# Kernel optimization log

Measured on AMD Instinct MI355X. Metric: run time of the kernel, lower is better.

## Reference

```python
import jax, jax.numpy as jnp
import numpy as np

B, S, D = 2, 2048, 4096
NH, NKV = 32, 8
HD = D // NH          # 128
NREP = NH // NKV      # 4
SCALE = HD ** -0.5


def setup_inputs() -> dict:
    key = jax.random.key(0)
    kx, kq, kk, kv, ko = jax.random.split(key, 5)
    s = 0.02
    return {
        "x": jax.random.normal(kx, (B, S, D), dtype=jnp.float32),
        "wq": jax.random.normal(kq, (D, NH * HD), dtype=jnp.float32) * s,
        "wk": jax.random.normal(kk, (D, NKV * HD), dtype=jnp.float32) * s,
        "wv": jax.random.normal(kv, (D, NKV * HD), dtype=jnp.float32) * s,
        "wo": jax.random.normal(ko, (NH * HD, D), dtype=jnp.float32) * s,
    }


def reference(x, wq, wk, wv, wo):
    b, s, _ = x.shape
    q = (x @ wq).reshape(b, s, NH, HD)    # b s h d
    k = (x @ wk).reshape(b, s, NKV, HD)   # b s kv d
    v = (x @ wv).reshape(b, s, NKV, HD)
    # GQA: repeat kv heads to match query heads
    k = jnp.repeat(k, NREP, axis=2)       # b s h d
    v = jnp.repeat(v, NREP, axis=2)
    scores = jnp.einsum("bihd,bjhd->bhij", q, k) * SCALE  # b h i j
    causal = jnp.tril(jnp.ones((s, s), dtype=bool))
    scores = jnp.where(causal, scores, jnp.finfo(scores.dtype).min)
    attn = jax.nn.softmax(scores, axis=-1)
    out = jnp.einsum("bhij,bjhd->bihd", attn, v)          # b s h d
    out = out.reshape(b, s, NH * HD)
    return out @ wo
```

## Files before the change

kernel.cpp:

```cpp
#include <hip/hip_runtime.h>
#include <cstdint>
#include <cstddef>

typedef __bf16 bf16x8 __attribute__((ext_vector_type(8)));
typedef float  f32x4  __attribute__((ext_vector_type(4)));
typedef unsigned short u16;

#define SCALE_F 0.08838834764831845f
#define QSCALE_F (0.08838834764831845f * 1.4426950408889634f)

__device__ __forceinline__ u16 f2bf(float f) {
  unsigned int u = __builtin_bit_cast(unsigned int, f);
  u += 0x7fffu + ((u >> 16) & 1u);
  return (u16)(u >> 16);
}

__device__ __forceinline__ unsigned cvt_pk_bf16(float lo, float hi) {
  unsigned r;
  asm("v_cvt_pk_bf16_f32 %0, %1, %2" : "=v"(r) : "v"(lo), "v"(hi));
  return r;
}

__device__ __forceinline__ void load_lds16(const void* g, void* l) {
  __builtin_amdgcn_global_load_lds((const __attribute__((address_space(1))) void*)g,
                                   (__attribute__((address_space(3))) void*)l,
                                   16, 0, 0);
}

__global__ __launch_bounds__(256) void prep_all(const float* __restrict__ x,
                                                const float* __restrict__ wq,
                                                const float* __restrict__ wk,
                                                const float* __restrict__ wv,
                                                const float* __restrict__ wo,
                                                u16* __restrict__ xb,
                                                u16* __restrict__ wqT,
                                                u16* __restrict__ wkvT,
                                                u16* __restrict__ woT) {
  __shared__ float tile[64][33];
  const int tid = threadIdx.x;
  int blk = blockIdx.x;
  if (blk < 2048) {
    int idx = blk * 256 + tid;
    const int n4 = 4096 * 4096 / 4;
    for (; idx < n4; idx += 2048 * 256) {
      float4 v = ((const float4*)x)[idx];
      uint2 pk;
      pk.x = (unsigned)f2bf(v.x) | ((unsigned)f2bf(v.y) << 16);
      pk.y = (unsigned)f2bf(v.z) | ((unsigned)f2bf(v.w) << 16);
      ((uint2*)xb)[idx] = pk;
    }
    return;
  }
  blk -= 2048;
  const float* in; u16* out; long C; int nbx; float scale;
  if (blk < 8192)       { in = wq; out = wqT;                           C = 4096; nbx = 128; scale = QSCALE_F; }
  else if (blk < 10240) { blk -= 8192;  in = wk; out = wkvT;                          C = 1024; nbx = 32; scale = 1.f; }
  else if (blk < 12288) { blk -= 10240; in = wv; out = wkvT + (size_t)1024 * 4096;    C = 1024; nbx = 32; scale = 1.f; }
  else                  { blk -= 12288; in = wo; out = woT;                           C = 4096; nbx = 128; scale = 1.f; }
  const long R = 4096;
  const long c0 = (long)(blk % nbx) * 32, r0 = (long)(blk / nbx) * 64;
  {
    const int tx = tid & 31, ty = tid >> 5;
#pragma unroll
    for (int i = 0; i < 8; i++)
      tile[ty + i * 8][tx] = in[(r0 + ty + i * 8) * C + c0 + tx];
  }
  __syncthreads();
  {
    const int tx = tid & 31, cy = tid >> 5;
#pragma unroll
    for (int i = 0; i < 4; i++) {
      int col = cy + i * 8;
      unsigned val = (unsigned)f2bf(tile[2 * tx][col] * scale) |
                     ((unsigned)f2bf(tile[2 * tx + 1][col] * scale) << 16);
      *(unsigned*)&out[(c0 + col) * R + r0 + 2 * tx] = val;
    }
  }
}

__global__ __launch_bounds__(256) void transpose_u16(const u16* __restrict__ in,
                                                     u16* __restrict__ out,
                                                     int R, int C, int ldi, int ldo) {
  __shared__ u16 tile[32][33];
  const int tx = threadIdx.x, ty = threadIdx.y;
  const long c0 = (long)blockIdx.x * 32, r0 = (long)blockIdx.y * 32;
#pragma unroll
  for (int i = 0; i < 4; i++)
    tile[ty + i * 8][tx] = in[(r0 + ty + i * 8) * (long)ldi + c0 + tx];
  __syncthreads();
#pragma unroll
  for (int i = 0; i < 4; i++)
    out[(c0 + ty + i * 8) * (long)ldo + r0 + tx] = tile[tx][ty + i * 8];
}

__global__ __launch_bounds__(256) void reduce_kv(const float* __restrict__ part,
                                                 u16* __restrict__ kvb, int n4) {
  int idx = blockIdx.x * 256 + threadIdx.x;
  const int stride = gridDim.x * 256;
  const float4* p0 = (const float4*)part;
  const float4* p1 = (const float4*)(part + (size_t)4096 * 2048);
  for (; idx < n4; idx += stride) {
    float4 a = p0[idx], b = p1[idx];
    uint2 pk;
    pk.x = (unsigned)f2bf(a.x + b.x) | ((unsigned)f2bf(a.y + b.y) << 16);
    pk.y = (unsigned)f2bf(a.z + b.z) | ((unsigned)f2bf(a.w + b.w) << 16);
    ((uint2*)kvb)[idx] = pk;
  }
}

#define STGA(db, ks, KC) { int kc_ = (KC) < K ? (KC) : 0; \
    load_lds16(gA0 + kc_, &SA[db][ks][s0 * 8]); \
    load_lds16(gA1 + kc_, &SA[db][ks][s1 * 8]); }
#define STGB(db, ks, KC) { int kc_ = (KC) < K ? (KC) : 0; \
    load_lds16(gB0 + kc_, &SB[db][ks][s0 * 8]); \
    load_lds16(gB1 + kc_, &SB[db][ks][s1 * 8]); }

#define PH(MBc, AU, BU, DBn, KSn, MBn, AN, RDB, BN_, STG, DOVM) { \
    STG; \
    if (DOVM) asm volatile("s_waitcnt vmcnt(8)"); \
    __builtin_amdgcn_s_barrier(); \
    _Pragma("unroll") for (int mm = 0; mm < 4; mm++) \
      AN[mm] = *(const bf16x8*)(&SA[DBn][KSn][aoff + (MBn + mm) * 512]); \
    if (RDB) { \
      _Pragma("unroll") for (int n = 0; n < 4; n++) \
        BN_[n] = *(const bf16x8*)(&SB[DBn][KSn][boff + n * 512]); \
    } \
    __builtin_amdgcn_s_setprio(1); \
    _Pragma("unroll") for (int mm = 0; mm < 4; mm++) \
      _Pragma("unroll") for (int n = 0; n < 4; n++) \
        acc[MBc + mm][n] = __builtin_amdgcn_mfma_f32_16x16x32_bf16(AU[mm], BU[n], acc[MBc + mm][n], 0, 0, 0); \
    __builtin_amdgcn_s_setprio(0); \
  }

template <int BF16_OUT>
__device__ __forceinline__ void gemm_core(const u16* __restrict__ A,
                                          const u16* __restrict__ Bt,
                                          void* __restrict__ Cv,
                                          long bm, long bn,
                                          int N, int K, int lda, int ldb) {
  __shared__ u16 SA[2][2][8192];
  __shared__ u16 SB[2][2][8192];
  const int tid = threadIdx.x;
  const int lane = tid & 63;
  const int g = lane >> 4, r16 = lane & 15;
  const int wid = tid >> 6;
  const int wm = wid >> 2, wn = wid & 3;

  const int s0 = tid, s1 = 512 + tid;
  const int rp0 = s0 >> 3, ci0 = (s0 & 7) ^ (rp0 & 7);
  const int rp1 = s1 >> 3, ci1 = (s1 & 7) ^ (rp1 & 7);
  const long gr0 = rp0 * 2 + (ci0 >> 2), gc0 = (ci0 & 3) * 8;
  const long gr1 = rp1 * 2 + (ci1 >> 2), gc1 = (ci1 & 3) * 8;
  const u16* gA0 = A + (bm + gr0) * lda + gc0;
  const u16* gA1 = A + (bm + gr1) * lda + gc1;
  const u16* gB0 = Bt + (bn + gr0) * ldb + gc0;
  const u16* gB1 = Bt + (bn + gr1) * ldb + gc1;

  const int rA = wm * 128 + r16;
  const int aoff = (rA >> 1) * 64 + ((((rA & 1) << 2) + g) ^ ((rA >> 1) & 7)) * 8;
  const int rB = wn * 64 + r16;
  const int boff = (rB >> 1) * 64 + ((((rB & 1) << 2) + g) ^ ((rB >> 1) & 7)) * 8;

  f32x4 acc[8][4];
#pragma unroll
  for (int m = 0; m < 8; m++)
#pragma unroll
    for (int n = 0; n < 4; n++)
#pragma unroll
      for (int j = 0; j < 4; j++) acc[m][n][j] = 0.f;

  bf16x8 afrX[4], afrY[4], bfrX[4], bfrY[4];

  STGA(0, 0, 0); STGB(0, 0, 0);
  STGA(0, 1, 32); STGB(0, 1, 32);
  STGA(1, 0, 64); STGB(1, 0, 64);
  __builtin_amdgcn_sched_barrier(0);
  asm volatile("s_waitcnt vmcnt(0)" ::: "memory");
  __builtin_amdgcn_s_barrier();

#pragma unroll
  for (int mm = 0; mm < 4; mm++)
    afrX[mm] = *(const bf16x8*)(&SA[0][0][aoff + mm * 512]);
#pragma unroll
  for (int n = 0; n < 4; n++)
    bfrX[n] = *(const bf16x8*)(&SB[0][0][boff + n * 512]);

  for (int it = 0; it < K / 128; it++) {
    const int t0 = it * 128;
    PH(0, afrX, bfrX, 0, 0, 4, afrY, 0, bfrY, STGA(1, 1, t0 + 96), 0);
    PH(4, afrY, bfrX, 0, 1, 0, afrX, 1, bfrY, STGB(1, 1, t0 + 96), 1);
    PH(0, afrX, bfrY, 0, 1, 4, afrY, 0, bfrX, STGA(0, 0, t0 + 128), 0);
    PH(4, afrY, bfrY, 1, 0, 0, afrX, 1, bfrX, STGB(0, 0, t0 + 128), 1);
    PH(0, afrX, bfrX, 1, 0, 4, afrY, 0, bfrY, STGA(0, 1, t0 + 160), 0);
    PH(4, afrY, bfrX, 1, 1, 0, afrX, 1, bfrY, STGB(0, 1, t0 + 160), 1);
    PH(0, afrX, bfrY, 1, 1, 4, afrY, 0, bfrX, STGA(1, 0, t0 + 192), 0);
    PH(4, afrY, bfrY, 0, 0, 0, afrX, 1, bfrX, STGB(1, 0, t0 + 192), 1);
  }

  const long crow = bm + wm * 128 + g * 4;
  const long ccol = bn + wn * 64 + r16;
  if (BF16_OUT) {
    u16* C = (u16*)Cv;
#pragma unroll
    for (int m = 0; m < 8; m++)
#pragma unroll
      for (int n = 0; n < 4; n++)
#pragma unroll
        for (int j = 0; j < 4; j++)
          C[(crow + m * 16 + j) * (long)N + ccol + n * 16] = f2bf(acc[m][n][j]);
  } else {
    float* C = (float*)Cv;
#pragma unroll
    for (int m = 0; m < 8; m++)
#pragma unroll
      for (int n = 0; n < 4; n++)
#pragma unroll
        for (int j = 0; j < 4; j++)
          C[(crow + m * 16 + j) * (long)N + ccol + n * 16] = acc[m][n][j];
  }
}

__global__ __launch_bounds__(512, 2) void gemm_q(const u16* __restrict__ A,
                                                 const u16* __restrict__ Bt,
                                                 void* __restrict__ Cv) {
  const int cpx = gridDim.x >> 3;
  const int lin = ((int)blockIdx.x & 7) * cpx + ((int)blockIdx.x >> 3);
  gemm_core<1>(A, Bt, Cv, (long)(lin / 16) * 256, (long)(lin % 16) * 256,
               4096, 4096, 4096, 4096);
}

__global__ __launch_bounds__(512, 2) void gemm_kv(const u16* __restrict__ A,
                                                  const u16* __restrict__ Bt,
                                                  float* __restrict__ part) {
  const int cpx = gridDim.x >> 3;
  const int lin = ((int)blockIdx.x & 7) * cpx + ((int)blockIdx.x >> 3);
  const int sk = lin >> 7;
  const int t = lin & 127;
  gemm_core<0>(A + sk * 2048, Bt + sk * 2048,
               part + (size_t)sk * 4096 * 2048,
               (long)(t >> 3) * 256, (long)(t & 7) * 256,
               2048, 2048, 4096, 4096);
}

__global__ __launch_bounds__(512, 2) void gemm_wo(const u16* __restrict__ A,
                                                  const u16* __restrict__ Bt,
                                                  void* __restrict__ Cv) {
  const int cpx = gridDim.x >> 3;
  const int lin = ((int)blockIdx.x & 7) * cpx + ((int)blockIdx.x >> 3);
  gemm_core<0>(A, Bt, Cv, (long)(lin / 16) * 256, (long)(lin % 16) * 256,
               4096, 4096, 4096, 4096);
}

#define ATILE(CUR, I, PREF) do { \
    const int kt_ = ((I) < nktA) ? (I) : (I) - nktA; \
    const int kb_ = kt_ * 64; \
    if (PREF) { \
      const int in_ = (I) + 1; \
      const int ktn_ = (in_ < nktA) ? in_ : in_ - nktA; \
      stage(CUR ^ 1, ktn_ * 64); \
    } \
    if (kb_ <= qlo + 15) { \
      const bool masked_ = (kb_ + 63 > qlo); \
      f32x4 st[4]; \
      _Pragma("unroll") for (int t = 0; t < 4; t++) \
        _Pragma("unroll") for (int j = 0; j < 4; j++) st[t][j] = 0.f; \
      _Pragma("unroll") for (int t = 0; t < 4; t++) \
        _Pragma("unroll") for (int kc = 0; kc < 4; kc++) { \
          bf16x8 kf = *(const bf16x8*)(kaK[CUR][kc & 1] + t * 2048 + (kc >> 1) * 64); \
          st[t] = __builtin_amdgcn_mfma_f32_16x16x32_bf16(kf, qf[kc], st[t], 0, 0, 0); \
        } \
      float p[4][4], tm[4]; \
      _Pragma("unroll") for (int t = 0; t < 4; t++) { \
        _Pragma("unroll") for (int j = 0; j < 4; j++) { \
          float s = st[t][j]; \
          if (masked_) { \
            int kv = kb_ + t * 16 + g * 4 + j; \
            s = (kv > qrow) ? -__builtin_inff() : s; \
          } \
          p[t][j] = s; \
        } \
        tm[t] = fmaxf(fmaxf(p[t][0], p[t][1]), fmaxf(p[t][2], p[t][3])); \
      } \
      float tmax = fmaxf(fmaxf(tm[0], tm[1]), fmaxf(tm[2], tm[3])); \
      tmax = fmaxf(tmax, __shfl_xor(tmax, 16)); \
      tmax = fmaxf(tmax, __shfl_xor(tmax, 32)); \
      if (!__all(tmax <= mrun + 8.f)) { \
        const float mnew = fmaxf(mrun, tmax); \
        const float esc = exp2f(mrun - mnew); \
        float es[4]; \
        _Pragma("unroll") for (int j = 0; j < 4; j++) es[j] = __shfl(esc, (lane & 48) + g * 4 + j); \
        _Pragma("unroll") for (int dt = 0; dt < 8; dt++) \
          _Pragma("unroll") for (int j = 0; j < 4; j++) oacc[dt][j] *= es[j]; \
        lrun *= esc; \
        mrun = mnew; \
      } \
      float ps01 = 0.f, ps23 = 0.f; \
      _Pragma("unroll") for (int t = 0; t < 4; t++) \
        _Pragma("unroll") for (int j = 0; j < 4; j++) { \
          float e = exp2f(p[t][j] - mrun); \
          p[t][j] = e; \
          if (t < 2) ps01 += e; else ps23 += e; \
        } \
      float psum = ps01 + ps23; \
      psum += __shfl_xor(psum, 16); \
      psum += __shfl_xor(psum, 32); \
      lrun += psum; \
      _Pragma("unroll") for (int t = 0; t < 4; t++) \
        _Pragma("unroll") for (int pp = 0; pp < 2; pp++) \
          *pwp32[t * 2 + pp] = cvt_pk_bf16(p[t][pp * 2], p[t][pp * 2 + 1]); \
      _Pragma("unroll") for (int kc2 = 0; kc2 < 2; kc2++) { \
        bf16x8 pa = *(const bf16x8*)(paP[kc2]); \
        _Pragma("unroll") for (int dt = 0; dt < 8; dt++) { \
          bf16x8 vf = *(const bf16x8*)(vaV[CUR][kc2] + dt * 1024); \
          oacc[dt] = __builtin_amdgcn_mfma_f32_16x16x32_bf16(pa, vf, oacc[dt], 0, 0, 0); \
        } \
      } \
    } \
    __syncthreads(); \
  } while (0)

__global__ __launch_bounds__(512, 4) void attn_fwd(const u16* __restrict__ Q,
                                                   const u16* __restrict__ KV,
                                                   const u16* __restrict__ VT,
                                                   u16* __restrict__ Og) {
  __shared__ u16 Ks[2][64 * 128];
  __shared__ u16 Vs[2][128 * 64];
  __shared__ u16 Ps[8][16 * 64];
  const int tid = threadIdx.x;
  const int lane = tid & 63;
  const int w = tid >> 6;
  const int g = lane >> 4, r16 = lane & 15;

  const int lin = ((int)blockIdx.x & 7) * 64 + ((int)blockIdx.x >> 3);
  const int b = lin >> 8;
  const int rem = lin & 255;
  const int kvh = rem >> 5;
  const int hrep = (rem & 31) >> 3;
  const int qtA = rem & 7;
  const int qtB = 15 - qtA;
  const int h = kvh * 4 + hrep;

  const u16* kcol   = KV + (long)b * 2048 * 2048 + kvh * 128;
  const u16* vb_ptr = VT + (long)kvh * 128 * 4096 + (long)b * 2048;
  u16* pw = Ps[w];

  const int nktA = 2 * (qtA + 1);
  const int ntot = 34;

  int qbase = qtA * 128;
  int qlo = qbase + w * 16;
  int qrow = qlo + r16;

  const int swz = r16 & 7;
  const u16* kaK[2][2];
  const u16* vaV[2][2];
  const u16* paP[2];
  unsigned* pwp32[8];
#pragma unroll
  for (int c2 = 0; c2 < 2; c2++) {
#pragma unroll
    for (int v = 0; v < 2; v++) {
      kaK[c2][v] = &Ks[c2][r16 * 128 + ((swz ^ (g + v * 4)) * 8)];
      vaV[c2][v] = &Vs[c2][r16 * 64 + ((swz ^ (v * 4 + g)) * 8)];
    }
  }
#pragma unroll
  for (int v = 0; v < 2; v++)
    paP[v] = pw + r16 * 64 + ((swz ^ (v * 4 + g)) * 8);
#pragma unroll
  for (int t = 0; t < 4; t++)
#pragma unroll
    for (int pp = 0; pp < 2; pp++)
      pwp32[t * 2 + pp] = (unsigned*)((char*)pw + r16 * 128 +
                          (((t * 32 + g * 8 + pp * 4) ^ (swz << 4))));

  bf16x8 qf[4];
  auto load_q = [&]() {
    const u16* qp = Q + ((long)(b * 2048 + qrow)) * 4096 + h * 128 + g * 8;
#pragma unroll
    for (int kc = 0; kc < 4; kc++) qf[kc] = *(const bf16x8*)(qp + kc * 32);
  };
  load_q();

  f32x4 oacc[8];
  float mrun, lrun;
  auto reinit = [&]() {
#pragma unroll
    for (int dt = 0; dt < 8; dt++)
#pragma unroll
      for (int j = 0; j < 4; j++) oacc[dt][j] = 0.f;
    mrun = -__builtin_inff();
    lrun = 0.f;
  };
  reinit();

  auto finalize = [&]() {
    float li[4];
#pragma unroll
    for (int j = 0; j < 4; j++)
      li[j] = 1.f / __shfl(lrun, (lane & 48) + g * 4 + j);
    u16* op = Og + ((long)(b * 2048 + qbase + w * 16 + g * 4)) * 4096 + h * 128 + r16;
#pragma unroll
    for (int dt = 0; dt < 8; dt++)
#pragma unroll
      for (int j = 0; j < 4; j++)
        op[(long)j * 4096 + dt * 16] = f2bf(oacc[dt][j] * li[j]);
  };

  auto stage = [&](int bf, int kb) {
#pragma unroll
    for (int i = 0; i < 2; i++) {
      int slot = i * 512 + tid;
      int r = slot >> 4, cs = slot & 15;
      int ck = (cs & 8) | ((cs ^ r) & 7);
      load_lds16(kcol + (long)(kb + r) * 2048 + ck * 8, &Ks[bf][slot * 8]);
      int d = slot >> 3, c8 = slot & 7;
      int cv = (c8 ^ d) & 7;
      load_lds16(vb_ptr + (long)d * 4096 + kb + cv * 8, &Vs[bf][slot * 8]);
    }
  };

  stage(0, 0);
  __syncthreads();

  for (int i = 0; i < ntot; i += 2) {
    if (i == nktA) {
      finalize();
      qbase = qtB * 128;
      qlo = qbase + w * 16;
      qrow = qlo + r16;
      load_q();
      reinit();
    }
    ATILE(0, i, 1);
    ATILE(1, i + 1, (i + 2 < ntot));
  }

  finalize();
}

extern "C" void kernel_launch(void* const* d_in, const int* in_sizes, int n_in,
                              void* d_out, int out_size, void* d_ws, size_t ws_size,
                              hipStream_t stream) {
  (void)in_sizes; (void)n_in; (void)out_size; (void)ws_size;
  const float* x  = (const float*)d_in[0];
  const float* wq = (const float*)d_in[1];
  const float* wk = (const float*)d_in[2];
  const float* wv = (const float*)d_in[3];
  const float* wo = (const float*)d_in[4];
  float* out = (float*)d_out;

  u16* xb    = (u16*)d_ws;
  u16* wqT   = xb   + (size_t)4096 * 4096;
  u16* wkvT  = wqT  + (size_t)4096 * 4096;
  u16* woT   = wkvT + (size_t)2048 * 4096;
  u16* qb    = woT  + (size_t)4096 * 4096;
  u16* kvb   = qb   + (size_t)4096 * 4096;
  u16* vT    = kvb  + (size_t)4096 * 2048;
  u16* attn  = xb;

  prep_all<<<22528, 256, 0, stream>>>(x, wq, wk, wv, wo, xb, wqT, wkvT, woT);

  gemm_q<<<256, 512, 0, stream>>>(xb, wqT, qb);
  gemm_kv<<<256, 512, 0, stream>>>(xb, wkvT, out);
  reduce_kv<<<2048, 256, 0, stream>>>(out, kvb, 4096 * 2048 / 4);
  transpose_u16<<<dim3(32, 128), dim3(32, 8), 0, stream>>>(kvb + 1024, vT, 4096, 1024, 2048, 4096);

  attn_fwd<<<512, 512, 0, stream>>>(qb, kvb, vT, attn);

  gemm_wo<<<256, 512, 0, stream>>>(attn, woT, out);
}
```

Measured before the change: 509.3 us.

## Process both paired query tiles together so each staged K/V tile is reused

Result: slower. 531.0 us (+4.3%).

```diff
diff --git a/kernel.cpp b/kernel.cpp
--- a/kernel.cpp
+++ b/kernel.cpp
@@ -251,78 +251,86 @@
                4096, 4096, 4096, 4096);
 }
 
-#define ATILE(CUR, I, PREF) do { \
-    const int kt_ = ((I) < nktA) ? (I) : (I) - nktA; \
-    const int kb_ = kt_ * 64; \
-    if (PREF) { \
-      const int in_ = (I) + 1; \
-      const int ktn_ = (in_ < nktA) ? in_ : in_ - nktA; \
-      stage(CUR ^ 1, ktn_ * 64); \
+#define SMUNIT(CUR, KB, QLO, QROW, QF, MRUN, LRUN, OACC) \
+  if ((KB) <= (QLO) + 15) { \
+    const bool masked_ = ((KB) + 63 > (QLO)); \
+    f32x4 st[4]; \
+    _Pragma("unroll") for (int t = 0; t < 4; t++) \
+      _Pragma("unroll") for (int j = 0; j < 4; j++) st[t][j] = 0.f; \
+    _Pragma("unroll") for (int t = 0; t < 4; t++) \
+      _Pragma("unroll") for (int kc = 0; kc < 4; kc++) { \
+        bf16x8 kf = *(const bf16x8*)(kaK[CUR][kc & 1] + t * 2048 + (kc >> 1) * 64); \
+        st[t] = __builtin_amdgcn_mfma_f32_16x16x32_bf16(kf, QF[kc], st[t], 0, 0, 0); \
+      } \
+    float p[4][4], tm[4]; \
+    _Pragma("unroll") for (int t = 0; t < 4; t++) { \
+      _Pragma("unroll") for (int j = 0; j < 4; j++) { \
+        float s = st[t][j]; \
+        if (masked_) { \
+          int kv = (KB) + t * 16 + g * 4 + j; \
+          s = (kv > (QROW)) ? -__builtin_inff() : s; \
+        } \
+        p[t][j] = s; \
+      } \
+      tm[t] = fmaxf(fmaxf(p[t][0], p[t][1]), fmaxf(p[t][2], p[t][3])); \
     } \
-    if (kb_ <= qlo + 15) { \
-      const bool masked_ = (kb_ + 63 > qlo); \
-      f32x4 st[4]; \
-      _Pragma("unroll") for (int t = 0; t < 4; t++) \
-        _Pragma("unroll") for (int j = 0; j < 4; j++) st[t][j] = 0.f; \
-      _Pragma("unroll") for (int t = 0; t < 4; t++) \
-        _Pragma("unroll") for (int kc = 0; kc < 4; kc++) { \
-          bf16x8 kf = *(const bf16x8*)(kaK[CUR][kc & 1] + t * 2048 + (kc >> 1) * 64); \
-          st[t] = __builtin_amdgcn_mfma_f32_16x16x32_bf16(kf, qf[kc], st[t], 0, 0, 0); \
-        } \
-      float p[4][4], tm[4]; \
-      _Pragma("unroll") for (int t = 0; t < 4; t++) { \
-        _Pragma("unroll") for (int j = 0; j < 4; j++) { \
-          float s = st[t][j]; \
-          if (masked_) { \
-            int kv = kb_ + t * 16 + g * 4 + j; \
-            s = (kv > qrow) ? -__builtin_inff() : s; \
-          } \
-          p[t][j] = s; \
-        } \
-        tm[t] = fmaxf(fmaxf(p[t][0], p[t][1]), fmaxf(p[t][2], p[t][3])); \
+    float tmax = fmaxf(fmaxf(tm[0], tm[1]), fmaxf(tm[2], tm[3])); \
+    tmax = fmaxf(tmax, __shfl_xor(tmax, 16)); \
+    tmax = fmaxf(tmax, __shfl_xor(tmax, 32)); \
+    if (!__all(tmax <= MRUN + 8.f)) { \
+      const float mnew = fmaxf(MRUN, tmax); \
+      const float esc = exp2f(MRUN - mnew); \
+      float es[4]; \
+      _Pragma("unroll") for (int j = 0; j < 4; j++) es[j] = __shfl(esc, (lane & 48) + g * 4 + j); \
+      _Pragma("unroll") for (int dt = 0; dt < 8; dt++) \
+        _Pragma("unroll") for (int j = 0; j < 4; j++) OACC[dt][j] *= es[j]; \
+      LRUN *= esc; \
+      MRUN = mnew; \
+    } \
+    float psum = 0.f; \
+    _Pragma("unroll") for (int t = 0; t < 4; t++) \
+      _Pragma("unroll") for (int j = 0; j < 4; j++) { \
+        float e = exp2f(p[t][j] - MRUN); \
+        p[t][j] = e; \
+        psum += e; \
       } \
-      float tmax = fmaxf(fmaxf(tm[0], tm[1]), fmaxf(tm[2], tm[3])); \
-      tmax = fmaxf(tmax, __shfl_xor(tmax, 16)); \
-      tmax = fmaxf(tmax, __shfl_xor(tmax, 32)); \
-      if (!__all(tmax <= mrun + 8.f)) { \
-        const float mnew = fmaxf(mrun, tmax); \
-        const float esc = exp2f(mrun - mnew); \
-        float es[4]; \
-        _Pragma("unroll") for (int j = 0; j < 4; j++) es[j] = __shfl(esc, (lane & 48) + g * 4 + j); \
-        _Pragma("unroll") for (int dt = 0; dt < 8; dt++) \
-          _Pragma("unroll") for (int j = 0; j < 4; j++) oacc[dt][j] *= es[j]; \
-        lrun *= esc; \
-        mrun = mnew; \
-      } \
-      float ps01 = 0.f, ps23 = 0.f; \
-      _Pragma("unroll") for (int t = 0; t < 4; t++) \
-        _Pragma("unroll") for (int j = 0; j < 4; j++) { \
-          float e = exp2f(p[t][j] - mrun); \
-          p[t][j] = e; \
-          if (t < 2) ps01 += e; else ps23 += e; \
-        } \
-      float psum = ps01 + ps23; \
-      psum += __shfl_xor(psum, 16); \
-      psum += __shfl_xor(psum, 32); \
-      lrun += psum; \
-      _Pragma("unroll") for (int t = 0; t < 4; t++) \
-        _Pragma("unroll") for (int pp = 0; pp < 2; pp++) \
-          *pwp32[t * 2 + pp] = cvt_pk_bf16(p[t][pp * 2], p[t][pp * 2 + 1]); \
-      _Pragma("unroll") for (int kc2 = 0; kc2 < 2; kc2++) { \
-        bf16x8 pa = *(const bf16x8*)(paP[kc2]); \
-        _Pragma("unroll") for (int dt = 0; dt < 8; dt++) { \
-          bf16x8 vf = *(const bf16x8*)(vaV[CUR][kc2] + dt * 1024); \
-          oacc[dt] = __builtin_amdgcn_mfma_f32_16x16x32_bf16(pa, vf, oacc[dt], 0, 0, 0); \
-        } \
+    psum += __shfl_xor(psum, 16); \
+    psum += __shfl_xor(psum, 32); \
+    LRUN += psum; \
+    _Pragma("unroll") for (int t = 0; t < 4; t++) \
+      _Pragma("unroll") for (int pp = 0; pp < 2; pp++) \
+        *pwp32[t * 2 + pp] = cvt_pk_bf16(p[t][pp * 2], p[t][pp * 2 + 1]); \
+    _Pragma("unroll") for (int kc2 = 0; kc2 < 2; kc2++) { \
+      bf16x8 pa = *(const bf16x8*)(paP[kc2]); \
+      _Pragma("unroll") for (int dt = 0; dt < 8; dt++) { \
+        bf16x8 vf = *(const bf16x8*)(vaV[CUR][kc2] + dt * 1024); \
+        OACC[dt] = __builtin_amdgcn_mfma_f32_16x16x32_bf16(pa, vf, OACC[dt], 0, 0, 0); \
       } \
     } \
+  }
+
+#define ATILE2(CUR, KT, PREF) do { \
+    const int kb_ = (KT) * 64; \
+    if (PREF) stage((CUR) ^ 1, kb_ + 64); \
+    SMUNIT(CUR, kb_, qloA, qrowA, qfA, mrunA, lrunA, oaccA) \
+    SMUNIT(CUR, kb_, qloB, qrowB, qfB, mrunB, lrunB, oaccB) \
     __syncthreads(); \
   } while (0)
 
-__global__ __launch_bounds__(512, 4) void attn_fwd(const u16* __restrict__ Q,
-                                                   const u16* __restrict__ KV,
-                                                   const u16* __restrict__ VT,
-                                                   u16* __restrict__ Og) {
+#define FINAL(QBASE, LRUN, OACC) { \
+    float li[4]; \
+    _Pragma("unroll") for (int j = 0; j < 4; j++) \
+      li[j] = 1.f / __shfl(LRUN, (lane & 48) + g * 4 + j); \
+    u16* op = Og + ((long)(b * 2048 + (QBASE) + w * 16 + g * 4)) * 4096 + h * 128 + r16; \
+    _Pragma("unroll") for (int dt = 0; dt < 8; dt++) \
+      _Pragma("unroll") for (int j = 0; j < 4; j++) \
+        op[(long)j * 4096 + dt * 16] = f2bf(OACC[dt][j] * li[j]); \
+  }
+
+__global__ __launch_bounds__(512) void attn_fwd(const u16* __restrict__ Q,
+                                                const u16* __restrict__ KV,
+                                                const u16* __restrict__ VT,
+                                                u16* __restrict__ Og) {
   __shared__ u16 Ks[2][64 * 128];
   __shared__ u16 Vs[2][128 * 64];
   __shared__ u16 Ps[8][16 * 64];
@@ -345,11 +353,12 @@
   u16* pw = Ps[w];
 
   const int nktA = 2 * (qtA + 1);
-  const int ntot = 34;
-
-  int qbase = qtA * 128;
-  int qlo = qbase + w * 16;
-  int qrow = qlo + r16;
+  const int nktB = 2 * (qtB + 1);
+
+  const int qbaseA = qtA * 128, qbaseB = qtB * 128;
+  const int qloA = qbaseA + w * 16, qloB = qbaseB + w * 16;
+  const int qrowA = qloA + r16, qrowB = qloB + r16;
+  (void)nktA;
 
   const int swz = r16 & 7;
   const u16* kaK[2][2];
@@ -374,38 +383,24 @@
       pwp32[t * 2 + pp] = (unsigned*)((char*)pw + r16 * 128 +
                           (((t * 32 + g * 8 + pp * 4) ^ (swz << 4))));
 
-  bf16x8 qf[4];
-  auto load_q = [&]() {
-    const u16* qp = Q + ((long)(b * 2048 + qrow)) * 4096 + h * 128 + g * 8;
-#pragma unroll
-    for (int kc = 0; kc < 4; kc++) qf[kc] = *(const bf16x8*)(qp + kc * 32);
-  };
-  load_q();
-
-  f32x4 oacc[8];
-  float mrun, lrun;
-  auto reinit = [&]() {
-#pragma unroll
-    for (int dt = 0; dt < 8; dt++)
-#pragma unroll
-      for (int j = 0; j < 4; j++) oacc[dt][j] = 0.f;
-    mrun = -__builtin_inff();
-    lrun = 0.f;
-  };
-  reinit();
-
-  auto finalize = [&]() {
-    float li[4];
-#pragma unroll
-    for (int j = 0; j < 4; j++)
-      li[j] = 1.f / __shfl(lrun, (lane & 48) + g * 4 + j);
-    u16* op = Og + ((long)(b * 2048 + qbase + w * 16 + g * 4)) * 4096 + h * 128 + r16;
-#pragma unroll
-    for (int dt = 0; dt < 8; dt++)
-#pragma unroll
-      for (int j = 0; j < 4; j++)
-        op[(long)j * 4096 + dt * 16] = f2bf(oacc[dt][j] * li[j]);
-  };
+  bf16x8 qfA[4], qfB[4];
+  {
+    const u16* qpA = Q + ((long)(b * 2048 + qrowA)) * 4096 + h * 128 + g * 8;
+    const u16* qpB = Q + ((long)(b * 2048 + qrowB)) * 4096 + h * 128 + g * 8;
+#pragma unroll
+    for (int kc = 0; kc < 4; kc++) {
+      qfA[kc] = *(const bf16x8*)(qpA + kc * 32);
+      qfB[kc] = *(const bf16x8*)(qpB + kc * 32);
+    }
+  }
+
+  f32x4 oaccA[8], oaccB[8];
+  float mrunA = -__builtin_inff(), lrunA = 0.f;
+  float mrunB = -__builtin_inff(), lrunB = 0.f;
+#pragma unroll
+  for (int dt = 0; dt < 8; dt++)
+#pragma unroll
+    for (int j = 0; j < 4; j++) { oaccA[dt][j] = 0.f; oaccB[dt][j] = 0.f; }
 
   auto stage = [&](int bf, int kb) {
 #pragma unroll
@@ -423,20 +418,13 @@
   stage(0, 0);
   __syncthreads();
 
-  for (int i = 0; i < ntot; i += 2) {
-    if (i == nktA) {
-      finalize();
-      qbase = qtB * 128;
-      qlo = qbase + w * 16;
-      qrow = qlo + r16;
-      load_q();
-      reinit();
-    }
-    ATILE(0, i, 1);
-    ATILE(1, i + 1, (i + 2 < ntot));
-  }
-
-  finalize();
+  for (int kt = 0; kt < nktB; kt += 2) {
+    ATILE2(0, kt, 1);
+    ATILE2(1, kt + 1, (kt + 2 < nktB));
+  }
+
+  FINAL(qbaseA, lrunA, oaccA);
+  FINAL(qbaseB, lrunB, oaccB);
 }
 
 extern "C" void kernel_launch(void* const* d_in, const int* in_sizes, int n_in,
```
